# Kernel optimization log

Hardware: AMD Instinct MI355X
Metric: run time of the kernel (lower is better)

The kernel has to match this reference:

```python
import jax, jax.numpy as jnp
import numpy as np

N_NODES, N_EDGES, NUM_GRAPHS = 50000, 800000, 64
F_DIM, H_DIM, N_LAYERS, N_CLASSES = 64, 64, 3, 16
EPS = 1e-5  # StdAggregation epsilon (PyG)


def setup_inputs() -> dict:
    key = jax.random.key(0)
    ks = jax.random.split(key, 12)
    s = 0.05
    x = jax.random.normal(ks[0], (N_NODES, F_DIM), jnp.float32)
    edge_index = jax.random.randint(ks[1], (2, N_EDGES), 0, N_NODES, dtype=jnp.int32)
    batch = jnp.sort(jax.random.randint(ks[2], (N_NODES,), 0, NUM_GRAPHS, dtype=jnp.int32))
    # per-layer PNAConv params (towers=1): pre Linear(2F->F), post Linear(13F->H), lin Linear(H->H)
    pre_w = jax.random.normal(ks[3], (N_LAYERS, F_DIM, 2 * F_DIM), jnp.float32) * s
    pre_b = jnp.zeros((N_LAYERS, F_DIM), jnp.float32)
    post_w = jax.random.normal(ks[4], (N_LAYERS, H_DIM, 13 * F_DIM), jnp.float32) * s
    post_b = jnp.zeros((N_LAYERS, H_DIM), jnp.float32)
    lin_w = jax.random.normal(ks[5], (N_LAYERS, H_DIM, H_DIM), jnp.float32) * s
    lin_b = jnp.zeros((N_LAYERS, H_DIM), jnp.float32)
    mlp_w1 = jax.random.normal(ks[6], (H_DIM, H_DIM), jnp.float32) * s
    mlp_b1 = jnp.zeros((H_DIM,), jnp.float32)
    mlp_w2 = jax.random.normal(ks[7], (N_CLASSES, H_DIM), jnp.float32) * s
    mlp_b2 = jnp.zeros((N_CLASSES,), jnp.float32)
    return dict(x=x, edge_index=edge_index, batch=batch,
                pre_w=pre_w, pre_b=pre_b, post_w=post_w, post_b=post_b,
                lin_w=lin_w, lin_b=lin_b, mlp_w1=mlp_w1, mlp_b1=mlp_b1,
                mlp_w2=mlp_w2, mlp_b2=mlp_b2)


def pna_forward(x, src, dst, pre_w, pre_b, post_w, post_b, lin_w, lin_b,
                mlp_w1, mlp_b1, mlp_w2, mlp_b2, batch):
    N = x.shape[0]
    deg_raw = jax.ops.segment_sum(jnp.ones_like(src, jnp.float32), dst, N)  # in-degree [N]
    deg = jnp.maximum(deg_raw, 1.0)[:, None]
    # avg log degree (PNA avg_deg['log'] from the degree histogram of this graph)
    avg_log = jnp.mean(jnp.log(deg_raw + 1.0))
    log_deg = jnp.log(deg + 1.0)
    amp = log_deg / avg_log          # amplification scaler [N,1]
    att = avg_log / log_deg          # attenuation scaler [N,1]
    has_in = (deg_raw > 0)[:, None]

    for l in range(pre_w.shape[0]):
        h = jnp.concatenate([x[dst], x[src]], axis=-1)        # [E, 2F] (x_i, x_j)
        m = h @ pre_w[l].T + pre_b[l]                          # pre_nn message [E, F]
        s1 = jax.ops.segment_sum(m, dst, N)
        s2 = jax.ops.segment_sum(m * m, dst, N)
        mean = s1 / deg
        std = jnp.sqrt(jax.nn.relu(s2 / deg - mean * mean) + EPS)
        mn = jnp.where(has_in, jax.ops.segment_min(m, dst, N), 0.0)
        mx = jnp.where(has_in, jax.ops.segment_max(m, dst, N), 0.0)
        aggr = jnp.concatenate([mean, mn, mx, std], axis=-1)   # [N, 4F]
        out = jnp.concatenate([x, aggr, aggr * amp, aggr * att], axis=-1)  # [N, 13F]
        out = out @ post_w[l].T + post_b[l]                    # post_nn [N, H]
        x = jax.nn.relu(out @ lin_w[l].T + lin_b[l])           # conv.lin + outer ReLU

    # global mean pool over graphs
    counts = jnp.maximum(
        jax.ops.segment_sum(jnp.ones((N,), x.dtype), batch, NUM_GRAPHS), 1.0)
    g = jax.ops.segment_sum(x, batch, NUM_GRAPHS) / counts[:, None]  # [G, H]
    g = jax.nn.relu(g @ mlp_w1.T + mlp_b1)
    return g @ mlp_w2.T + mlp_b2                               # [G, C]


def reference(x, edge_index, batch, pre_w, pre_b, post_w, post_b,
              lin_w, lin_b, mlp_w1, mlp_b1, mlp_w2, mlp_b2):
    src, dst = edge_index[0], edge_index[1]
    return pna_forward(x, src, dst, pre_w, pre_b, post_w, post_b,
                       lin_w, lin_b, mlp_w1, mlp_b1, mlp_w2, mlp_b2, batch)
```

## Files before the change

kernel.cpp:

```cpp
#include <hip/hip_runtime.h>
#include <math.h>

#define N_NODES   50000
#define N_EDGES   800000
#define NUM_GRAPHS 64
#define FDIM      64
#define HDIM      64
#define NLAYERS   3
#define NCLASSES  16
#define EPS       1e-5f

#define SCAN_CHUNK 1024
#define NCHUNKS ((N_NODES + SCAN_CHUNK - 1) / SCAN_CHUNK)

typedef unsigned short u16;
typedef unsigned int   u32;
typedef __attribute__((ext_vector_type(8))) short short8;
typedef __attribute__((ext_vector_type(4))) float floatx4;

#define WKS_LAYER 159744
#define PRES_LAYER 24576
#define KPOST_LDS_BYTES 159744

__device__ inline void split1(float f, u16& h, u16& m, u16& l) {
    u32 b  = __float_as_uint(f);
    u32 hb = b & 0xFFFF0000u;
    float r = f - __uint_as_float(hb);
    u32 mb = __float_as_uint(r) & 0xFFFF0000u;
    float r2 = r - __uint_as_float(mb);
    u32 lb = __float_as_uint(r2) & 0xFFFF0000u;
    h = (u16)(hb >> 16); m = (u16)(mb >> 16); l = (u16)(lb >> 16);
}

__device__ inline void gl_lds16(const void* g, void* l) {
    __builtin_amdgcn_global_load_lds(
        (const __attribute__((address_space(1))) u32*)g,
        (__attribute__((address_space(3))) u32*)l, 16, 0, 0);
}

__global__ __launch_bounds__(256) void k_comb(const float* __restrict__ post_w,
                                              const float* __restrict__ lin_w,
                                              const float* __restrict__ pre_w,
                                              const float* __restrict__ post_b,
                                              const float* __restrict__ lin_b,
                                              u16* __restrict__ WkS,
                                              u16* __restrict__ PreS,
                                              float* __restrict__ bcv,
                                              int* __restrict__ cnt,
                                              float* __restrict__ logsum) {
    int b = blockIdx.x, t = threadIdx.x;
    int zi = b * 256 + t;
    if (zi < N_NODES) cnt[zi] = 0;
    if (zi == 0) *logsum = 0.f;

    if (b < 624) {
        int c  = t & 63;
        int kl = t >> 6;
        int l  = b / 208;
        int o  = (b % 208) * 4 + kl;
        const float* lw = lin_w + (size_t)l * 4096 + c * 64;
        const float* pw = post_w + (size_t)l * 53248 + o;
        float acc = 0.f;
        #pragma unroll 8
        for (int j = 0; j < 64; ++j)
            acc += lw[j] * pw[(size_t)j * 832];
        u16 h, m, lo;
        split1(acc, h, m, lo);

        int kn;
        if (o < 64) kn = o;
        else {
            int s  = (o - 64) >> 8;
            int mm = (o - 64) & 255;
            int j  = mm >> 5, r = mm & 31;
            kn = 64 + j * 96 + s * 32 + r;
        }
        int ch  = kn >> 5;
        int kin = kn & 31;
        int n16 = c & 15, nt = c >> 4;
        int swk = (((kin >> 3) + (n16 >> 1)) & 3) * 8 + (kin & 7);
        size_t base = (size_t)l * WKS_LAYER + (size_t)ch * 6144
                    + nt * 512 + n16 * 32 + swk;
        WkS[base]        = h;
        WkS[base + 2048] = m;
        WkS[base + 4096] = lo;
    } else if (b == 624) {
        if (t < 192) {
            int l = t >> 6, c = t & 63;
            float acc = lin_b[l * 64 + c];
            for (int j = 0; j < 64; ++j)
                acc += lin_w[(size_t)l * 4096 + c * 64 + j] * post_b[l * 64 + j];
            bcv[l * 64 + c] = acc;
        }
    } else {
        int i = (b - 625) * 256 + t;
        int l = i >> 13;
        int rem = i & 8191;
        int c128 = rem >> 6;
        int k = rem & 63;
        float v;
        if (c128 < 64) v = pre_w[(size_t)l * 8192 + c128 * 128 + k];
        else           v = pre_w[(size_t)l * 8192 + (c128 - 64) * 128 + 64 + k];
        u16 h, m, lo;
        split1(v, h, m, lo);
        int ch = k >> 5, kin = k & 31;
        int nt = c128 >> 4, n16 = c128 & 15;
        int swk = (((kin >> 3) + (n16 >> 1)) & 3) * 8 + (kin & 7);
        size_t base = (size_t)l * PRES_LAYER + (size_t)ch * 12288
                    + nt * 512 + n16 * 32 + swk;
        PreS[base]        = h;
        PreS[base + 4096] = m;
        PreS[base + 8192] = lo;
    }
}

__global__ void k_count(const int* __restrict__ dst, int* __restrict__ cnt,
                        int* __restrict__ rank) {
    int e = blockIdx.x * 256 + threadIdx.x;
    if (e < N_EDGES) rank[e] = atomicAdd(&cnt[dst[e]], 1);
}

__global__ void k_chunk_sums(const int* __restrict__ cnt, int* __restrict__ bsum,
                             float* __restrict__ logsum) {
    __shared__ int   ired[256];
    __shared__ float lred[256];
    int b = blockIdx.x, t = threadIdx.x;
    int base = b * SCAN_CHUNK;
    int s = 0; float ls = 0.f;
    for (int i = t; i < SCAN_CHUNK; i += 256) {
        int idx = base + i;
        if (idx < N_NODES) {
            int v = cnt[idx];
            s += v;
            ls += logf((float)v + 1.0f);
        }
    }
    ired[t] = s; lred[t] = ls;
    __syncthreads();
    for (int off = 128; off > 0; off >>= 1) {
        if (t < off) { ired[t] += ired[t + off]; lred[t] += lred[t + off]; }
        __syncthreads();
    }
    if (t == 0) { bsum[b] = ired[0]; atomicAdd(logsum, lred[0]); }
}

__global__ void k_scan_top(const int* __restrict__ bsum, int* __restrict__ boff,
                           int* __restrict__ row_start) {
    if (threadIdx.x == 0) {
        int acc = 0;
        for (int i = 0; i < NCHUNKS; ++i) { boff[i] = acc; acc += bsum[i]; }
        row_start[N_NODES] = acc;
    }
}

__global__ void k_scan_chunks(const int* __restrict__ cnt, const int* __restrict__ boff,
                              int* __restrict__ row_start) {
    __shared__ int tsum[256];
    int b = blockIdx.x, t = threadIdx.x;
    int base = b * SCAN_CHUNK + t * 4;
    int v[4]; int s = 0;
    #pragma unroll
    for (int i = 0; i < 4; ++i) {
        int idx = base + i;
        v[i] = (idx < N_NODES) ? cnt[idx] : 0;
        s += v[i];
    }
    tsum[t] = s;
    __syncthreads();
    for (int off = 1; off < 256; off <<= 1) {
        int val = (t >= off) ? tsum[t - off] : 0;
        __syncthreads();
        tsum[t] += val;
        __syncthreads();
    }
    int excl = boff[b] + tsum[t] - s;
    #pragma unroll
    for (int i = 0; i < 4; ++i) {
        int idx = base + i;
        if (idx < N_NODES) row_start[idx] = excl;
        excl += v[i];
    }
}

__global__ void k_scatter(const int* __restrict__ src, const int* __restrict__ dst,
                          const int* __restrict__ rank,
                          const int* __restrict__ row_start,
                          int* __restrict__ csr_src) {
    int e = blockIdx.x * 256 + threadIdx.x;
    if (e < N_EDGES) {
        int d = dst[e];
        csr_src[row_start[d] + rank[e]] = src[e];
    }
}

__global__ void k_scal(const int* __restrict__ cnt, const float* __restrict__ logsum,
                       float* __restrict__ inv_deg, float* __restrict__ ampv,
                       float* __restrict__ attv, float* __restrict__ g_sum,
                       int* __restrict__ g_cnt) {
    int n = blockIdx.x * 256 + threadIdx.x;
    if (blockIdx.x == 0) {
        for (int i = threadIdx.x; i < 4096; i += 256) g_sum[i] = 0.f;
        if (threadIdx.x < 64) g_cnt[threadIdx.x] = 0;
    }
    if (n < N_NODES) {
        float avg = logsum[0] / (float)N_NODES;
        float degf = fmaxf((float)cnt[n], 1.0f);
        inv_deg[n] = 1.0f / degf;
        float ld = logf(degf + 1.0f);
        ampv[n] = ld / avg;
        attv[n] = avg / ld;
    }
}

__global__ __launch_bounds__(256, 4) void k_pre(const float* __restrict__ x,
                                                const u16* __restrict__ PreS,
                                                const float* __restrict__ pre_b,
                                                float* __restrict__ p,
                                                float* __restrict__ q) {
    __shared__ u16 ldsB[2 * 12288];
    int t = threadIdx.x;
    int w = t >> 6;
    int lane = t & 63;
    int m = lane & 15;
    int qh = lane >> 4;
    int rowBase = blockIdx.x * 64;

    int myrow = rowBase + 16 * w + m;
    bool vr = myrow < N_NODES;
    int crow = vr ? myrow : 0;
    const float* xrow = x + (size_t)crow * 64;

    int bo = m * 32 + ((qh + (m >> 1)) & 3) * 8;

    #pragma unroll
    for (int ch = 0; ch < 2; ++ch) {
        const char* g = (const char*)PreS + (size_t)ch * 24576 + w * 6144 + lane * 16;
        char* l = (char*)ldsB + ch * 24576 + w * 6144;
        #pragma unroll
        for (int i = 0; i < 6; ++i)
            gl_lds16(g + i * 1024, l + i * 1024);
    }
    float fa[2][8];
    #pragma unroll
    for (int ch = 0; ch < 2; ++ch) {
        const float* sp = xrow + ch * 32 + qh * 8;
        float4 u0 = *(const float4*)sp;
        float4 u1 = *(const float4*)(sp + 4);
        fa[ch][0] = vr ? u0.x : 0.f; fa[ch][1] = vr ? u0.y : 0.f;
        fa[ch][2] = vr ? u0.z : 0.f; fa[ch][3] = vr ? u0.w : 0.f;
        fa[ch][4] = vr ? u1.x : 0.f; fa[ch][5] = vr ? u1.y : 0.f;
        fa[ch][6] = vr ? u1.z : 0.f; fa[ch][7] = vr ? u1.w : 0.f;
    }
    asm volatile("s_waitcnt vmcnt(0)" ::: "memory");
    __syncthreads();

    floatx4 acc[8] = {};
    #pragma unroll
    for (int ch = 0; ch < 2; ++ch) {
        union { u32 u[4]; short8 s8; } AH, AM, AL;
        #pragma unroll
        for (int i = 0; i < 4; ++i) {
            float f0 = fa[ch][2 * i], f1 = fa[ch][2 * i + 1];
            u32 b0 = __float_as_uint(f0), b1 = __float_as_uint(f1);
            u32 h0 = b0 & 0xFFFF0000u,  h1 = b1 & 0xFFFF0000u;
            float r0 = f0 - __uint_as_float(h0);
            float r1 = f1 - __uint_as_float(h1);
            u32 m0 = __float_as_uint(r0) & 0xFFFF0000u;
            u32 m1 = __float_as_uint(r1) & 0xFFFF0000u;
            float s0 = r0 - __uint_as_float(m0);
            float s1 = r1 - __uint_as_float(m1);
            u32 l0 = __float_as_uint(s0) & 0xFFFF0000u;
            u32 l1 = __float_as_uint(s1) & 0xFFFF0000u;
            AH.u[i] = (h0 >> 16) | h1;
            AM.u[i] = (m0 >> 16) | m1;
            AL.u[i] = (l0 >> 16) | l1;
        }
        const u16* Bb = ldsB + ch * 12288;
        #pragma unroll
        for (int nt = 0; nt < 8; ++nt) {
            short8 bH = *(const short8*)(Bb + nt * 512 + bo);
            short8 bM = *(const short8*)(Bb + 4096 + nt * 512 + bo);
            short8 bL = *(const short8*)(Bb + 8192 + nt * 512 + bo);
            acc[nt] = __builtin_amdgcn_mfma_f32_16x16x32_bf16(AH.s8, bH, acc[nt], 0, 0, 0);
            acc[nt] = __builtin_amdgcn_mfma_f32_16x16x32_bf16(AH.s8, bM, acc[nt], 0, 0, 0);
            acc[nt] = __builtin_amdgcn_mfma_f32_16x16x32_bf16(AM.s8, bH, acc[nt], 0, 0, 0);
            acc[nt] = __builtin_amdgcn_mfma_f32_16x16x32_bf16(AH.s8, bL, acc[nt], 0, 0, 0);
            acc[nt] = __builtin_amdgcn_mfma_f32_16x16x32_bf16(AM.s8, bM, acc[nt], 0, 0, 0);
            acc[nt] = __builtin_amdgcn_mfma_f32_16x16x32_bf16(AL.s8, bH, acc[nt], 0, 0, 0);
        }
    }

    int col = m;
    #pragma unroll
    for (int nt = 0; nt < 8; ++nt) {
        int cbase = (nt & 3) * 16 + col;
        float bias = (nt < 4) ? pre_b[cbase] : 0.f;
        float* outp = (nt < 4) ? p : q;
        #pragma unroll
        for (int reg = 0; reg < 4; ++reg) {
            int grow = rowBase + 16 * w + qh * 4 + reg;
            if (grow < N_NODES)
                outp[(size_t)grow * 64 + cbase] = acc[nt][reg] + bias;
        }
    }
}

__global__ __launch_bounds__(256) void k_aggr(const float* __restrict__ p,
                                              const float* __restrict__ q,
                                              const int* __restrict__ row_start,
                                              const int* __restrict__ csr_src,
                                              const float* __restrict__ inv_deg,
                                              float* __restrict__ aggr) {
    int wid  = (blockIdx.x * 256 + threadIdx.x) >> 6;
    int lane = threadIdx.x & 63;
    if (wid >= N_NODES) return;
    int n = wid;
    int beg = row_start[n], end = row_start[n + 1];
    float sum = 0.f, sq = 0.f;
    float mn = INFINITY, mx = -INFINITY;
    int e = beg;
    for (; e + 7 < end; e += 8) {
        float qv[8];
        #pragma unroll
        for (int u = 0; u < 8; ++u) {
            int s = csr_src[e + u];
            qv[u] = q[(size_t)s * 64 + lane];
        }
        #pragma unroll
        for (int u = 0; u < 8; ++u) {
            float m = qv[u];
            sum += m; sq += m * m;
            mn = fminf(mn, m); mx = fmaxf(mx, m);
        }
    }
    for (; e + 3 < end; e += 4) {
        float qv[4];
        #pragma unroll
        for (int u = 0; u < 4; ++u) {
            int s = csr_src[e + u];
            qv[u] = q[(size_t)s * 64 + lane];
        }
        #pragma unroll
        for (int u = 0; u < 4; ++u) {
            float m = qv[u];
            sum += m; sq += m * m;
            mn = fminf(mn, m); mx = fmaxf(mx, m);
        }
    }
    for (; e < end; ++e) {
        int s = csr_src[e];
        float m = q[(size_t)s * 64 + lane];
        sum += m; sq += m * m;
        mn = fminf(mn, m); mx = fmaxf(mx, m);
    }
    float* a = aggr + (size_t)n * 256;
    if (end <= beg) {
        a[lane]       = 0.f;
        a[64 + lane]  = 0.f;
        a[128 + lane] = 0.f;
        a[192 + lane] = sqrtf(EPS);
    } else {
        float pv = p[n * 64 + lane];
        float id = inv_deg[n];
        float meanq = sum * id;
        float var = fmaxf(sq * id - meanq * meanq, 0.f);
        a[lane]       = pv + meanq;
        a[64 + lane]  = pv + mn;
        a[128 + lane] = pv + mx;
        a[192 + lane] = sqrtf(var + EPS);
    }
}

__global__ __launch_bounds__(512, 2) void k_post(const float* __restrict__ x,
                                                 const float* __restrict__ aggr,
                                                 const float* __restrict__ ampv,
                                                 const float* __restrict__ attv,
                                                 const u16* __restrict__ WkS,
                                                 const float* __restrict__ bc,
                                                 float* __restrict__ xout) {
    extern __shared__ u16 ldsB[];
    int t = threadIdx.x;
    int w = t >> 6;
    int lane = t & 63;
    int m = lane & 15;
    int qh = lane >> 4;
    int nh = blockIdx.x & 1;
    int rowBase = (blockIdx.x >> 1) * 256 + 32 * w;

    for (int u = w; u < 156; u += 8) {
        int ch = u / 6;
        int r  = u - ch * 6;
        int sp = r >> 1;
        int h2 = r & 1;
        const char* g = (const char*)WkS + ch * 12288 + sp * 4096
                      + nh * 2048 + h2 * 1024 + lane * 16;
        char* l = (char*)ldsB + u * 1024;
        gl_lds16(g, l);
    }

    int row0 = rowBase + m;
    int row1 = row0 + 16;
    int cr0 = (row0 < N_NODES) ? row0 : 0;
    int cr1 = (row1 < N_NODES) ? row1 : 0;
    const float* xr0 = x + (size_t)cr0 * 64;
    const float* xr1 = x + (size_t)cr1 * 64;
    const float* ar0 = aggr + (size_t)cr0 * 256;
    const float* ar1 = aggr + (size_t)cr1 * 256;

    int bo = m * 32 + ((qh + (m >> 1)) & 3) * 8;

    floatx4 accP0[2] = {}, accA0[2] = {}, accT0[2] = {};
    floatx4 accP1[2] = {}, accA1[2] = {}, accT1[2] = {};

    float f0[8], f1[8];
    union U8 { u32 u[4]; short8 s8; };
    U8 AH0, AM0, AL0, AH1, AM1, AL1;

    auto loadRaw = [&](const float* sp, float* f) {
        float4 u0 = *(const float4*)(sp + qh * 8);
        float4 u1 = *(const float4*)(sp + qh * 8 + 4);
        f[0] = u0.x; f[1] = u0.y; f[2] = u0.z; f[3] = u0.w;
        f[4] = u1.x; f[5] = u1.y; f[6] = u1.z; f[7] = u1.w;
    };
    auto split2 = [&](const float* f, U8& H, U8& M8, U8& L) {
        #pragma unroll
        for (int i = 0; i < 4; ++i) {
            float v0 = f[2 * i], v1 = f[2 * i + 1];
            u32 b0 = __float_as_uint(v0), b1 = __float_as_uint(v1);
            u32 h0 = b0 & 0xFFFF0000u,  h1 = b1 & 0xFFFF0000u;
            float r0 = v0 - __uint_as_float(h0);
            float r1 = v1 - __uint_as_float(h1);
            u32 m0 = __float_as_uint(r0) & 0xFFFF0000u;
            u32 m1 = __float_as_uint(r1) & 0xFFFF0000u;
            float s0 = r0 - __uint_as_float(m0);
            float s1 = r1 - __uint_as_float(m1);
            u32 l0 = __float_as_uint(s0) & 0xFFFF0000u;
            u32 l1 = __float_as_uint(s1) & 0xFFFF0000u;
            H.u[i]  = (h0 >> 16) | h1;
            M8.u[i] = (m0 >> 16) | m1;
            L.u[i]  = (l0 >> 16) | l1;
        }
    };
    auto chunkMM = [&](int ch, floatx4* A0, floatx4* A1) {
        const u16* pB = ldsB + ch * 3072 + bo;
        short8 bH[2], bM[2], bL[2];
        #pragma unroll
        for (int nt = 0; nt < 2; ++nt) {
            bH[nt] = *(const short8*)(pB + nt * 512);
            bM[nt] = *(const short8*)(pB + 1024 + nt * 512);
            bL[nt] = *(const short8*)(pB + 2048 + nt * 512);
        }
        #pragma unroll
        for (int nt = 0; nt < 2; ++nt) {
            A0[nt] = __builtin_amdgcn_mfma_f32_16x16x32_bf16(AH0.s8, bH[nt], A0[nt], 0, 0, 0);
            A0[nt] = __builtin_amdgcn_mfma_f32_16x16x32_bf16(AH0.s8, bM[nt], A0[nt], 0, 0, 0);
            A0[nt] = __builtin_amdgcn_mfma_f32_16x16x32_bf16(AM0.s8, bH[nt], A0[nt], 0, 0, 0);
            A0[nt] = __builtin_amdgcn_mfma_f32_16x16x32_bf16(AH0.s8, bL[nt], A0[nt], 0, 0, 0);
            A0[nt] = __builtin_amdgcn_mfma_f32_16x16x32_bf16(AM0.s8, bM[nt], A0[nt], 0, 0, 0);
            A0[nt] = __builtin_amdgcn_mfma_f32_16x16x32_bf16(AL0.s8, bH[nt], A0[nt], 0, 0, 0);
            A1[nt] = __builtin_amdgcn_mfma_f32_16x16x32_bf16(AH1.s8, bH[nt], A1[nt], 0, 0, 0);
            A1[nt] = __builtin_amdgcn_mfma_f32_16x16x32_bf16(AH1.s8, bM[nt], A1[nt], 0, 0, 0);
            A1[nt] = __builtin_amdgcn_mfma_f32_16x16x32_bf16(AM1.s8, bH[nt], A1[nt], 0, 0, 0);
            A1[nt] = __builtin_amdgcn_mfma_f32_16x16x32_bf16(AH1.s8, bL[nt], A1[nt], 0, 0, 0);
            A1[nt] = __builtin_amdgcn_mfma_f32_16x16x32_bf16(AM1.s8, bM[nt], A1[nt], 0, 0, 0);
            A1[nt] = __builtin_amdgcn_mfma_f32_16x16x32_bf16(AL1.s8, bH[nt], A1[nt], 0, 0, 0);
        }
    };

    loadRaw(xr0, f0); loadRaw(xr1, f1);
    asm volatile("s_waitcnt vmcnt(0)" ::: "memory");
    __syncthreads();

    split2(f0, AH0, AM0, AL0); split2(f1, AH1, AM1, AL1);
    loadRaw(xr0 + 32, f0); loadRaw(xr1 + 32, f1);
    chunkMM(0, accP0, accP1);
    split2(f0, AH0, AM0, AL0); split2(f1, AH1, AM1, AL1);
    loadRaw(ar0, f0); loadRaw(ar1, f1);
    chunkMM(1, accP0, accP1);
    for (int j = 0; j < 8; ++j) {
        split2(f0, AH0, AM0, AL0); split2(f1, AH1, AM1, AL1);
        if (j < 7) { loadRaw(ar0 + (j + 1) * 32, f0); loadRaw(ar1 + (j + 1) * 32, f1); }
        int ch = 2 + 3 * j;
        chunkMM(ch,     accP0, accP1);
        chunkMM(ch + 1, accA0, accA1);
        chunkMM(ch + 2, accT0, accT1);
    }

    int col = m;
    #pragma unroll
    for (int frag = 0; frag < 2; ++frag) {
        #pragma unroll
        for (int reg = 0; reg < 4; ++reg) {
            int grow = rowBase + 16 * frag + qh * 4 + reg;
            if (grow < N_NODES) {
                float av = ampv[grow], tv = attv[grow];
                #pragma unroll
                for (int nt = 0; nt < 2; ++nt) {
                    int cbase = (nh * 2 + nt) * 16 + col;
                    float pv  = frag ? accP1[nt][reg] : accP0[nt][reg];
                    float av2 = frag ? accA1[nt][reg] : accA0[nt][reg];
                    float tv2 = frag ? accT1[nt][reg] : accT0[nt][reg];
                    float v = pv + av * av2 + tv * tv2 + bc[cbase];
                    xout[(size_t)grow * 64 + cbase] = fmaxf(v, 0.f);
                }
            }
        }
    }
}

__global__ __launch_bounds__(256) void k_pool(const float* __restrict__ x,
                                              const int* __restrict__ batch,
                                              float* __restrict__ g_sum,
                                              int* __restrict__ g_cnt) {
    int lane = threadIdx.x & 63;
    int wave = blockIdx.x * 4 + (threadIdx.x >> 6);
    const int NPW = 16;
    int beg = wave * NPW;
    if (beg >= N_NODES) return;
    int end = min(beg + NPW, N_NODES);
    float acc = 0.f;
    int cur = batch[beg];
    int c = 0;
    for (int n = beg; n < end; ++n) {
        int b = batch[n];
        if (b != cur) {
            atomicAdd(&g_sum[cur * 64 + lane], acc);
            if (lane == 0) atomicAdd(&g_cnt[cur], c);
            acc = 0.f; c = 0; cur = b;
        }
        acc += x[n * 64 + lane];
        ++c;
    }
    atomicAdd(&g_sum[cur * 64 + lane], acc);
    if (lane == 0) atomicAdd(&g_cnt[cur], c);
}

__global__ __launch_bounds__(256) void k_mlp(const float* __restrict__ g_sum,
                                             const int* __restrict__ g_cnt,
                                             const float* __restrict__ w1,
                                             const float* __restrict__ b1,
                                             const float* __restrict__ w2,
                                             const float* __restrict__ b2,
                                             float* __restrict__ out) {
    __shared__ float g[64][64];
    __shared__ float h[64][64];
    __shared__ float wT[64][65];
    int t = threadIdx.x;
    for (int idx = t; idx < 4096; idx += 256) {
        int gi = idx >> 6, c = idx & 63;
        float cntf = fmaxf((float)g_cnt[gi], 1.f);
        g[gi][c] = g_sum[idx] / cntf;
    }
    for (int idx = t; idx < 4096; idx += 256) {
        int c = idx >> 6, k = idx & 63;
        wT[k][c] = w1[c * 64 + k];
    }
    __syncthreads();
    for (int idx = t; idx < 4096; idx += 256) {
        int gi = idx >> 6, c = idx & 63;
        float acc = b1[c];
        for (int k = 0; k < 64; ++k) acc += g[gi][k] * wT[k][c];
        h[gi][c] = fmaxf(acc, 0.f);
    }
    __syncthreads();
    for (int idx = t; idx < 64 * NCLASSES; idx += 256) {
        int gi = idx >> 4, c = idx & 15;
        float acc = b2[c];
        for (int k = 0; k < 64; ++k) acc += h[gi][k] * w2[c * 64 + k];
        out[gi * NCLASSES + c] = acc;
    }
}

extern "C" void kernel_launch(void* const* d_in, const int* in_sizes, int n_in,
                              void* d_out, int out_size, void* d_ws, size_t ws_size,
                              hipStream_t stream) {
    const float* x      = (const float*)d_in[0];
    const int*   ei     = (const int*)d_in[1];
    const int*   batch  = (const int*)d_in[2];
    const float* pre_w  = (const float*)d_in[3];
    const float* pre_b  = (const float*)d_in[4];
    const float* post_w = (const float*)d_in[5];
    const float* post_b = (const float*)d_in[6];
    const float* lin_w  = (const float*)d_in[7];
    const float* lin_b  = (const float*)d_in[8];
    const float* mlp_w1 = (const float*)d_in[9];
    const float* mlp_b1 = (const float*)d_in[10];
    const float* mlp_w2 = (const float*)d_in[11];
    const float* mlp_b2 = (const float*)d_in[12];

    const int* src = ei;
    const int* dst = ei + N_EDGES;

    char* base = (char*)d_ws;
    size_t off = 0;
    auto alloc = [&](size_t bytes) -> void* {
        void* ptr = base + off;
        off += (bytes + 255) & ~(size_t)255;
        return ptr;
    };
    int*   cnt       = (int*)alloc(N_NODES * 4);
    int*   row_start = (int*)alloc((N_NODES + 1) * 4);
    int*   rank      = (int*)alloc(N_EDGES * 4);
    int*   csr_src   = (int*)alloc(N_EDGES * 4);
    int*   bsum      = (int*)alloc(64 * 4);
    int*   boff      = (int*)alloc(64 * 4);
    float* logsum    = (float*)alloc(16);
    float* inv_deg   = (float*)alloc(N_NODES * 4);
    float* ampv      = (float*)alloc(N_NODES * 4);
    float* attv      = (float*)alloc(N_NODES * 4);
    float* p         = (float*)alloc((size_t)N_NODES * 64 * 4);
    float* q         = (float*)alloc((size_t)N_NODES * 64 * 4);
    float* aggr      = (float*)alloc((size_t)N_NODES * 256 * 4);
    float* xb0       = (float*)alloc((size_t)N_NODES * 64 * 4);
    float* xb1       = (float*)alloc((size_t)N_NODES * 64 * 4);
    float* g_sum     = (float*)alloc(64 * 64 * 4);
    int*   g_cnt     = (int*)alloc(64 * 4);
    u16*   WkS       = (u16*)alloc((size_t)3 * WKS_LAYER * 2);
    u16*   PreS      = (u16*)alloc((size_t)3 * PRES_LAYER * 2);
    float* bcv       = (float*)alloc(3 * 64 * 4);

    k_comb<<<721, 256, 0, stream>>>(post_w, lin_w, pre_w, post_b, lin_b,
                                    WkS, PreS, bcv, cnt, logsum);

    k_count<<<(N_EDGES + 255) / 256, 256, 0, stream>>>(dst, cnt, rank);
    k_chunk_sums<<<NCHUNKS, 256, 0, stream>>>(cnt, bsum, logsum);
    k_scan_top<<<1, 64, 0, stream>>>(bsum, boff, row_start);
    k_scan_chunks<<<NCHUNKS, 256, 0, stream>>>(cnt, boff, row_start);
    k_scatter<<<(N_EDGES + 255) / 256, 256, 0, stream>>>(src, dst, rank,
                                                         row_start, csr_src);
    k_scal<<<(N_NODES + 255) / 256, 256, 0, stream>>>(cnt, logsum, inv_deg,
                                                      ampv, attv, g_sum, g_cnt);

    const int PRE_BLOCKS  = (N_NODES + 63) / 64;
    const int POST_BLOCKS = 2 * ((N_NODES + 255) / 256);
    const float* xin = x;
    float* bufs[3] = {xb0, xb1, xb0};
    for (int l = 0; l < NLAYERS; ++l) {
        k_pre<<<PRE_BLOCKS, 256, 0, stream>>>(xin, PreS + (size_t)l * PRES_LAYER,
                                              pre_b + l * 64, p, q);
        k_aggr<<<(N_NODES + 3) / 4, 256, 0, stream>>>(p, q, row_start, csr_src,
                                                      inv_deg, aggr);
        float* xo = bufs[l];
        k_post<<<POST_BLOCKS, 512, KPOST_LDS_BYTES, stream>>>(
            xin, aggr, ampv, attv, WkS + (size_t)l * WKS_LAYER,
            bcv + l * 64, xo);
        xin = xo;
    }

    int pool_waves = (N_NODES + 15) / 16;
    k_pool<<<(pool_waves + 3) / 4, 256, 0, stream>>>(xin, batch, g_sum, g_cnt);
    k_mlp<<<1, 256, 0, stream>>>(g_sum, g_cnt, mlp_w1, mlp_b1, mlp_w2, mlp_b2,
                                 (float*)d_out);
}
```

Baseline: 464.8 us.

## Double post-kernel block rows and interleave MFMA accumulator chains

Raises the k_post block size from 512 to 1024 threads, so each block covers 512 node rows. The ~156 KB weight tile staged into LDS is then reused across twice as many rows, halving the per-row cost of filling it. The split-precision MFMA sequence is reordered to alternate across the four independent accumulators instead of running six dependent MFMAs back to back on one. The launch bound (1024,4) may push the compiler to cap registers tightly and spill, since LDS use already limits each CU to one block.

```diff
diff --git a/kernel.cpp b/kernel.cpp
--- a/kernel.cpp
+++ b/kernel.cpp
@@ -371,13 +371,13 @@
     }
 }
 
-__global__ __launch_bounds__(512, 2) void k_post(const float* __restrict__ x,
-                                                 const float* __restrict__ aggr,
-                                                 const float* __restrict__ ampv,
-                                                 const float* __restrict__ attv,
-                                                 const u16* __restrict__ WkS,
-                                                 const float* __restrict__ bc,
-                                                 float* __restrict__ xout) {
+__global__ __launch_bounds__(1024, 4) void k_post(const float* __restrict__ x,
+                                                  const float* __restrict__ aggr,
+                                                  const float* __restrict__ ampv,
+                                                  const float* __restrict__ attv,
+                                                  const u16* __restrict__ WkS,
+                                                  const float* __restrict__ bc,
+                                                  float* __restrict__ xout) {
     extern __shared__ u16 ldsB[];
     int t = threadIdx.x;
     int w = t >> 6;
@@ -385,9 +385,9 @@
     int m = lane & 15;
     int qh = lane >> 4;
     int nh = blockIdx.x & 1;
-    int rowBase = (blockIdx.x >> 1) * 256 + 32 * w;
-
-    for (int u = w; u < 156; u += 8) {
+    int rowBase = (blockIdx.x >> 1) * 512 + 32 * w;
+
+    for (int u = w; u < 156; u += 16) {
         int ch = u / 6;
         int r  = u - ch * 6;
         int sp = r >> 1;
@@ -441,30 +441,21 @@
             L.u[i]  = (l0 >> 16) | l1;
         }
     };
+    #define MF(A, B, C) C = __builtin_amdgcn_mfma_f32_16x16x32_bf16((A).s8, (B), (C), 0, 0, 0)
     auto chunkMM = [&](int ch, floatx4* A0, floatx4* A1) {
         const u16* pB = ldsB + ch * 3072 + bo;
-        short8 bH[2], bM[2], bL[2];
-        #pragma unroll
-        for (int nt = 0; nt < 2; ++nt) {
-            bH[nt] = *(const short8*)(pB + nt * 512);
-            bM[nt] = *(const short8*)(pB + 1024 + nt * 512);
-            bL[nt] = *(const short8*)(pB + 2048 + nt * 512);
-        }
-        #pragma unroll
-        for (int nt = 0; nt < 2; ++nt) {
-            A0[nt] = __builtin_amdgcn_mfma_f32_16x16x32_bf16(AH0.s8, bH[nt], A0[nt], 0, 0, 0);
-            A0[nt] = __builtin_amdgcn_mfma_f32_16x16x32_bf16(AH0.s8, bM[nt], A0[nt], 0, 0, 0);
-            A0[nt] = __builtin_amdgcn_mfma_f32_16x16x32_bf16(AM0.s8, bH[nt], A0[nt], 0, 0, 0);
-            A0[nt] = __builtin_amdgcn_mfma_f32_16x16x32_bf16(AH0.s8, bL[nt], A0[nt], 0, 0, 0);
-            A0[nt] = __builtin_amdgcn_mfma_f32_16x16x32_bf16(AM0.s8, bM[nt], A0[nt], 0, 0, 0);
-            A0[nt] = __builtin_amdgcn_mfma_f32_16x16x32_bf16(AL0.s8, bH[nt], A0[nt], 0, 0, 0);
-            A1[nt] = __builtin_amdgcn_mfma_f32_16x16x32_bf16(AH1.s8, bH[nt], A1[nt], 0, 0, 0);
-            A1[nt] = __builtin_amdgcn_mfma_f32_16x16x32_bf16(AH1.s8, bM[nt], A1[nt], 0, 0, 0);
-            A1[nt] = __builtin_amdgcn_mfma_f32_16x16x32_bf16(AM1.s8, bH[nt], A1[nt], 0, 0, 0);
-            A1[nt] = __builtin_amdgcn_mfma_f32_16x16x32_bf16(AH1.s8, bL[nt], A1[nt], 0, 0, 0);
-            A1[nt] = __builtin_amdgcn_mfma_f32_16x16x32_bf16(AM1.s8, bM[nt], A1[nt], 0, 0, 0);
-            A1[nt] = __builtin_amdgcn_mfma_f32_16x16x32_bf16(AL1.s8, bH[nt], A1[nt], 0, 0, 0);
-        }
+        short8 bH0 = *(const short8*)(pB);
+        short8 bH1 = *(const short8*)(pB + 512);
+        short8 bM0 = *(const short8*)(pB + 1024);
+        short8 bM1 = *(const short8*)(pB + 1536);
+        short8 bL0 = *(const short8*)(pB + 2048);
+        short8 bL1 = *(const short8*)(pB + 2560);
+        MF(AH0, bH0, A0[0]); MF(AH1, bH0, A1[0]); MF(AH0, bH1, A0[1]); MF(AH1, bH1, A1[1]);
+        MF(AH0, bM0, A0[0]); MF(AH1, bM0, A1[0]); MF(AH0, bM1, A0[1]); MF(AH1, bM1, A1[1]);
+        MF(AM0, bH0, A0[0]); MF(AM1, bH0, A1[0]); MF(AM0, bH1, A0[1]); MF(AM1, bH1, A1[1]);
+        MF(AH0, bL0, A0[0]); MF(AH1, bL0, A1[0]); MF(AH0, bL1, A0[1]); MF(AH1, bL1, A1[1]);
+        MF(AM0, bM0, A0[0]); MF(AM1, bM0, A1[0]); MF(AM0, bM1, A0[1]); MF(AM1, bM1, A1[1]);
+        MF(AL0, bH0, A0[0]); MF(AL1, bH0, A1[0]); MF(AL0, bH1, A0[1]); MF(AL1, bH1, A1[1]);
     };
 
     loadRaw(xr0, f0); loadRaw(xr1, f1);
@@ -485,6 +476,7 @@
         chunkMM(ch + 1, accA0, accA1);
         chunkMM(ch + 2, accT0, accT1);
     }
+    #undef MF
 
     int col = m;
     #pragma unroll
@@ -632,7 +624,7 @@
                                                       ampv, attv, g_sum, g_cnt);
 
     const int PRE_BLOCKS  = (N_NODES + 63) / 64;
-    const int POST_BLOCKS = 2 * ((N_NODES + 255) / 256);
+    const int POST_BLOCKS = 2 * ((N_NODES + 511) / 512);
     const float* xin = x;
     float* bufs[3] = {xb0, xb1, xb0};
     for (int l = 0; l < NLAYERS; ++l) {
@@ -641,7 +633,7 @@
         k_aggr<<<(N_NODES + 3) / 4, 256, 0, stream>>>(p, q, row_start, csr_src,
                                                       inv_deg, aggr);
         float* xo = bufs[l];
-        k_post<<<POST_BLOCKS, 512, KPOST_LDS_BYTES, stream>>>(
+        k_post<<<POST_BLOCKS, 1024, KPOST_LDS_BYTES, stream>>>(
             xin, aggr, ampv, attv, WkS + (size_t)l * WKS_LAYER,
             bcv + l * 64, xo);
         xin = xo;
```

New measurement: 453.1 us. 2.5% less time.
